# Optimization experiments

Hardware: AMD Instinct MI355X
Metric: run time of the kernel (lower is better)

The kernel has to match this reference:

```python
import jax, jax.numpy as jnp
import numpy as np

B, R, P, DP, DR, N, RK = 4, 256, 64, 384, 512, 48, 24


def _ln(x, w, b, eps=1e-5):
    m = x.mean(-1, keepdims=True)
    v = ((x - m) ** 2).mean(-1, keepdims=True)
    return (x - m) / jnp.sqrt(v + eps) * w + b


def _l2norm(x, eps=1e-6):
    return x / jnp.maximum(jnp.linalg.norm(x, axis=-1, keepdims=True), eps)


def setup_inputs() -> dict:
    key = jax.random.key(0)
    ks = jax.random.split(key, 16)
    s = 0.02
    rnd = lambda k, shp: jax.random.normal(k, shp, jnp.float32) * s
    inp = {
        'patch_tokens': jax.random.normal(ks[0], (B, R, P, DP), jnp.float32),
        'patch_mask': jax.random.randint(ks[1], (B, R, P), 0, 2) > 0,
        'near_mask': jax.random.randint(ks[2], (R, R), 0, 2) > 0,
        'far_mask': jax.random.randint(ks[3], (R, R), 0, 2) > 0,
        'local_pos': rnd(ks[4], (1, 1, P, DP)),
        'gate_ln_w': jnp.ones(DP), 'gate_ln_b': jnp.zeros(DP),
        'gate_w1': rnd(ks[5], (DP, DR)), 'gate_b1': jnp.zeros(DR),
        'gate_w2': rnd(ks[6], (DR, 1)), 'gate_b2': jnp.zeros(1),
        'proj_ln1_w': jnp.ones(DP), 'proj_ln1_b': jnp.zeros(DP),
        'proj_w1': rnd(ks[7], (DP, DR)), 'proj_b1': jnp.zeros(DR),
        'proj_w2': rnd(ks[8], (DR, DR)), 'proj_b2': jnp.zeros(DR),
        'proj_ln2_w': jnp.ones(DR), 'proj_ln2_b': jnp.zeros(DR),
        'in_proj_w': rnd(ks[9], (DR, 2 * DR)),
        'x_proj_w': rnd(ks[10], (DR, RK + 2 * N)),
        'dt_w': rnd(ks[11], (RK, DR)),
        'dt_b': jax.random.uniform(ks[12], (DR,), jnp.float32, -4.0, -2.0),
        'A_log': jnp.tile(jnp.log(jnp.arange(1, N + 1, dtype=jnp.float32))[None, :], (DR, 1)),
        'D_param': jnp.ones(DR),
        'out_proj_w': rnd(ks[13], (DR, DR)),
        'scan_ln_w': jnp.ones(DR), 'scan_ln_b': jnp.zeros(DR),
    }
    return inp


def _forward(patch_tokens, patch_mask, near_mask, far_mask, local_pos,
             gate_ln_w, gate_ln_b, gate_w1, gate_b1, gate_w2, gate_b2,
             proj_ln1_w, proj_ln1_b, proj_w1, proj_b1, proj_w2, proj_b2,
             proj_ln2_w, proj_ln2_b, in_proj_w, x_proj_w, dt_w, dt_b,
             A_log, D_param, out_proj_w, scan_ln_w, scan_ln_b):
    # ---- GatedRegionAggregator ----
    x = patch_tokens + local_pos  # [B,R,P,DP]
    g = _ln(x, gate_ln_w, gate_ln_b)
    g = jax.nn.gelu(g @ gate_w1 + gate_b1, approximate=False)
    logits = (g @ gate_w2 + gate_b2)[..., 0]  # [B,R,P]
    logits = jnp.where(patch_mask, logits, jnp.finfo(logits.dtype).min)
    attn = jax.nn.softmax(logits, axis=-1) * patch_mask
    attn = attn / jnp.maximum(attn.sum(-1, keepdims=True), 1e-6)
    pooled = jnp.einsum('brp,brpd->brd', attn, x)  # [B,R,DP]
    p = _ln(pooled, proj_ln1_w, proj_ln1_b)
    p = jax.nn.gelu(p @ proj_w1 + proj_b1, approximate=False)
    p = _ln(p @ proj_w2 + proj_b2, proj_ln2_w, proj_ln2_b)
    p = jnp.nan_to_num(p, nan=0.0, posinf=1.0, neginf=-1.0)
    region = _l2norm(p)  # [B,R,DR]

    # ---- SlowSelectiveScan1D over region sequence (L = R) ----
    xz = region @ in_proj_w  # [B,L,2*DR]
    u, z = jnp.split(xz, 2, axis=-1)
    prm = u @ x_proj_w  # [B,L,RK+2N]
    dt_raw, Bm, Cm = prm[..., :RK], prm[..., RK:RK + N], prm[..., RK + N:]
    delta = jnp.minimum(jax.nn.softplus(dt_raw @ dt_w + dt_b), 10.0)  # [B,L,DR]
    A = -jnp.minimum(jnp.exp(A_log), 1e4)  # [DR,N]
    dA = jnp.exp(jnp.clip(delta[..., None] * A[None, None], -30.0, 30.0))  # [B,L,DR,N]
    dBu = delta[..., None] * Bm[:, :, None, :] * u[..., None]  # [B,L,DR,N]
    log_cumA = jnp.cumsum(jnp.log(jnp.maximum(dA, 1e-38)), axis=1)
    h = jnp.exp(log_cumA) * jnp.cumsum(dBu * jnp.exp(-log_cumA), axis=1)
    y_seq = jnp.einsum('bln,bldn->bld', Cm, h) + D_param * u
    y = (y_seq * jax.nn.silu(z)) @ out_proj_w
    out = _ln(region + jnp.nan_to_num(y, nan=0.0, posinf=1.0, neginf=-1.0),
              scan_ln_w, scan_ln_b)  # [B,R,DR]

    # ---- topology_loss_static ----
    rt = _l2norm(out.astype(jnp.float32))
    sim = jnp.einsum('brd,bsd->brs', rt, rt)  # [B,R,R]
    near = near_mask.astype(sim.dtype)[None]
    far = far_mask.astype(sim.dtype)[None]
    near_loss = ((1.0 - sim) * near).sum() / jnp.maximum(near.sum(), 1.0)
    far_loss = (jax.nn.relu(sim - 0.2) * far).sum() / jnp.maximum(far.sum(), 1.0)
    return out, near_loss + far_loss


def reference(patch_tokens, patch_mask, near_mask, far_mask, local_pos,
              gate_ln_w, gate_ln_b, gate_w1, gate_b1, gate_w2, gate_b2,
              proj_ln1_w, proj_ln1_b, proj_w1, proj_b1, proj_w2, proj_b2,
              proj_ln2_w, proj_ln2_b, in_proj_w, x_proj_w, dt_w, dt_b,
              A_log, D_param, out_proj_w, scan_ln_w, scan_ln_b):
    return _forward(patch_tokens, patch_mask, near_mask, far_mask, local_pos,
                    gate_ln_w, gate_ln_b, gate_w1, gate_b1, gate_w2, gate_b2,
                    proj_ln1_w, proj_ln1_b, proj_w1, proj_b1, proj_w2, proj_b2,
                    proj_ln2_w, proj_ln2_b, in_proj_w, x_proj_w, dt_w, dt_b,
                    A_log, D_param, out_proj_w, scan_ln_w, scan_ln_b)
```

## Files before the change

kernel.cpp:

```cpp
#include <hip/hip_runtime.h>
#include <hip/hip_bf16.h>
#include <math.h>

#define B_ 4
#define R_ 256
#define P_ 64
#define DP_ 384
#define DR_ 512
#define N_ 48
#define RK_ 24
#define MROWS (B_*R_*P_)
#define REGS  (B_*R_)

typedef unsigned short ushort_t;
typedef __attribute__((ext_vector_type(8))) short bf16x8;
typedef __attribute__((ext_vector_type(4))) float f32x4;

#define GLOAD16(g, l) __builtin_amdgcn_global_load_lds( \
    (const __attribute__((address_space(1))) unsigned int*)(g), \
    (__attribute__((address_space(3))) unsigned int*)(l), 16, 0, 0)

#define OFF_PW1  0
#define OFF_PW2  196608
#define OFF_INPW 458752
#define OFF_XPW  983040
#define OFF_DTW  1044480
#define NW_TOT   1056768

__device__ __forceinline__ float us2f(unsigned short u){
  union { unsigned int i; float f; } x; x.i = ((unsigned int)u) << 16; return x.f;
}
__device__ __forceinline__ unsigned short f2us(float f){
  __hip_bfloat16 h = __float2bfloat16(f);
  return *reinterpret_cast<unsigned short*>(&h);
}
__device__ __forceinline__ float gelu_f(float x){
  float u = x * 0.70710678118654752f;
  float au = fabsf(u);
  float tt = 1.0f / fmaf(0.3275911f, au, 1.0f);
  float poly = tt * fmaf(tt, fmaf(tt, fmaf(tt, fmaf(tt, 1.061405429f, -1.453152027f),
                       1.421413741f), -0.284496736f), 0.254829592f);
  float erfv = 1.0f - poly * __expf(-au * au);
  erfv = (u < 0.f) ? -erfv : erfv;
  return 0.5f * x * (1.0f + erfv);
}
__device__ __forceinline__ float wred_sum(float v){
#pragma unroll
  for (int m = 1; m < 64; m <<= 1) v += __shfl_xor(v, m, 64);
  return v;
}
__device__ __forceinline__ void block_sum4(float v[4], float* s){
  int lane = threadIdx.x & 63, wid = threadIdx.x >> 6;
#pragma unroll
  for (int i = 0; i < 4; ++i){
    float x = v[i];
#pragma unroll
    for (int m = 1; m < 64; m <<= 1) x += __shfl_xor(x, m, 64);
    if (lane == 0) s[wid * 4 + i] = x;
  }
  __syncthreads();
  if (threadIdx.x < 4){
    float t = 0.f;
    for (int t2 = 0; t2 < 8; ++t2) t += s[t2 * 4 + threadIdx.x];
    s[32 + threadIdx.x] = t;
  }
  __syncthreads();
#pragma unroll
  for (int i = 0; i < 4; ++i) v[i] = s[32 + i];
  __syncthreads();
}
__device__ __forceinline__ void block_sum2(float& a, float& b, float* s){
  int lane = threadIdx.x & 63, wid = threadIdx.x >> 6;
  float x = a, y = b;
#pragma unroll
  for (int m = 1; m < 64; m <<= 1){ x += __shfl_xor(x, m, 64); y += __shfl_xor(y, m, 64); }
  if (lane == 0){ s[wid * 2] = x; s[wid * 2 + 1] = y; }
  __syncthreads();
  if (threadIdx.x < 2){
    float t = 0.f;
    for (int j = 0; j < 8; ++j) t += s[j * 2 + threadIdx.x];
    s[16 + threadIdx.x] = t;
  }
  __syncthreads();
  a = s[16]; b = s[17];
  __syncthreads();
}

__global__ __launch_bounds__(512) void k_prep(
    const float* __restrict__ gw1, const float* __restrict__ glnw,
    const float* __restrict__ glnb, const float* __restrict__ gb1,
    ushort_t* __restrict__ W1pT, float* __restrict__ s1,
    float* __restrict__ b1p, float* __restrict__ accum){
  __shared__ float pss[8][64], psb[8][64];
  int tid = threadIdx.x, seg = tid >> 6, nl = tid & 63;
  int n = blockIdx.x * 64 + nl;
  if (blockIdx.x == 0 && tid < 4) accum[tid] = 0.f;
  float s = 0.f, sb = 0.f;
  int k0 = seg * 48;
  for (int i = 0; i < 48; ++i){
    int k = k0 + i;
    float w1 = gw1[k * DR_ + n];
    float v = glnw[k] * w1;
    unsigned short vr = f2us(v);
    s  += us2f(vr);
    sb += glnb[k] * w1;
    W1pT[(size_t)n * DP_ + k] = vr;
  }
  pss[seg][nl] = s; psb[seg][nl] = sb;
  __syncthreads();
  if (tid < 64){
    float ts = 0.f, tb = 0.f;
    for (int j = 0; j < 8; ++j){ ts += pss[j][tid]; tb += psb[j][tid]; }
    s1[blockIdx.x * 64 + tid] = ts;
    b1p[blockIdx.x * 64 + tid] = gb1[blockIdx.x * 64 + tid] + tb;
  }
}

// ... 17 lines not shown
__global__ __launch_bounds__(512) void k_xform(
    const float* __restrict__ pt, const float* __restrict__ lp,
    ushort_t* __restrict__ xb, float* __restrict__ mu, float* __restrict__ rsg){
  int tid = threadIdx.x, w = tid >> 6, lane = tid & 63;
  size_t r = (size_t)blockIdx.x * 8 + w;
  int p = (int)(r & (P_ - 1));
  const float* xr = pt + r * DP_ + lane * 6;
  const float* lr = lp + (size_t)p * DP_ + lane * 6;
  float x[6];
  float s = 0.f, ss = 0.f;
#pragma unroll
  for (int i = 0; i < 6; i += 2){
    float2 a = *(const float2*)(xr + i);
    float2 b = *(const float2*)(lr + i);
    x[i] = a.x + b.x; x[i + 1] = a.y + b.y;
  }
#pragma unroll
  for (int i = 0; i < 6; ++i){ s += x[i]; ss += x[i] * x[i]; }
  s = wred_sum(s); ss = wred_sum(ss);
  if (lane == 0){
    float m = s * (1.f / DP_);
    float var = ss * (1.f / DP_) - m * m;
    mu[r] = m;
    rsg[r] = rsqrtf(var + 1e-5f);
  }
  ushort_t* xw = xb + r * DP_ + lane * 6;
#pragma unroll
  for (int i = 0; i < 6; i += 2){
    ushort2 u2; u2.x = f2us(x[i]); u2.y = f2us(x[i + 1]);
    *(ushort2*)(xw + i) = u2;
  }
}

__global__ __launch_bounds__(1024) void k_gate(
    const ushort_t* __restrict__ xb,
    const ushort_t* __restrict__ BT,
    const float* __restrict__ mu, const float* __restrict__ rsg,
    const float* __restrict__ s1, const float* __restrict__ b1p,
    const float* __restrict__ w2, float* __restrict__ logits){
  __shared__ __align__(16) ushort_t Abuf[2][128 * 64];
  __shared__ float logit_lds[128];
  __shared__ float smu[128], srs[128];
  int tid = threadIdx.x;
  int lane = tid & 63, w = tid >> 6;
  int t = lane & 15, g = lane >> 4;
  long r0 = (long)blockIdx.x * 128;
  if (tid < 128){
    logit_lds[tid] = 0.f;
    smu[tid] = mu[r0 + tid];
    srs[tid] = rsg[r0 + tid];
  }

  f32x4 acc[8][2];
#pragma unroll
  for (int m = 0; m < 8; ++m)
#pragma unroll
    for (int n = 0; n < 2; ++n) acc[m][n] = (f32x4){0.f, 0.f, 0.f, 0.f};

  int ro = lane >> 3, c = lane & 7;
  int srow = (w << 3) + ro;
  const ushort_t* asrc = xb + (size_t)(r0 + srow) * DP_ + ((c ^ (srow & 7)) << 3);

  GLOAD16(asrc, Abuf[0] + (w << 9));
  __syncthreads();

  for (int kt = 0; kt < 6; ++kt){
    int cb = kt & 1;
    if (kt < 5) GLOAD16(asrc + (kt + 1) * 64, Abuf[cb ^ 1] + (w << 9));
    bf16x8 bfr[2][2];
#pragma unroll
    for (int kk = 0; kk < 2; ++kk)
#pragma unroll
      for (int n = 0; n < 2; ++n){
        int col = w * 32 + n * 16 + t;
        bfr[kk][n] = *(const bf16x8*)(BT + (size_t)col * DP_ + kt * 64 + (kk * 4 + g) * 8);
      }
#pragma unroll
    for (int kk = 0; kk < 2; ++kk){
      int ch = kk * 4 + g;
#pragma unroll
      for (int m = 0; m < 8; ++m){
        int row = m * 16 + t;
        bf16x8 af = *(const bf16x8*)(Abuf[cb] + row * 64 + ((ch ^ (row & 7)) << 3));
#pragma unroll
        for (int n = 0; n < 2; ++n)
          acc[m][n] = __builtin_amdgcn_mfma_f32_16x16x32_bf16(af, bfr[kk][n], acc[m][n], 0, 0, 0);
      }
    }
    __syncthreads();
  }

  float w2c[2], s1c[2], b1c[2];
#pragma unroll
  for (int n = 0; n < 2; ++n){
    int col = w * 32 + n * 16 + t;
    w2c[n] = w2[col]; s1c[n] = s1[col]; b1c[n] = b1p[col];
  }
#pragma unroll
  for (int m = 0; m < 8; ++m){
#pragma unroll
    for (int j = 0; j < 4; ++j){
      int rl = m * 16 + g * 4 + j;
      float mur = smu[rl], rs = srs[rl];
      float part = 0.f;
#pragma unroll
      for (int n = 0; n < 2; ++n){
        float gp = rs * acc[m][n][j] - mur * rs * s1c[n] + b1c[n];
        part += gelu_f(gp) * w2c[n];
      }
#pragma unroll
      for (int msk = 1; msk < 16; msk <<= 1) part += __shfl_xor(part, msk, 64);
      if (t == 0) atomicAdd(&logit_lds[rl], part);
    }
  }
  __syncthreads();
  if (tid < 128) logits[r0 + tid] = logit_lds[tid];
}

__global__ __launch_bounds__(512) void k_pool(
    const ushort_t* __restrict__ xb, const float* __restrict__ logits,
    const int* __restrict__ pmask, float* __restrict__ pooled){
  __shared__ float attn[64];
  __shared__ float part[8][DP_];
  int tid = threadIdx.x;
  long r0 = (long)blockIdx.x * 64;
  if (tid < 64){
    int mk = pmask[r0 + tid];
    float lv = logits[r0 + tid];
    float lm = mk ? lv : -3.4e38f;
    float M = lm;
#pragma unroll
    for (int m2 = 1; m2 < 64; m2 <<= 1) M = fmaxf(M, __shfl_xor(M, m2, 64));
    float e = mk ? __expf(lv - M) : 0.f;
    float S = e;
#pragma unroll
    for (int m2 = 1; m2 < 64; m2 <<= 1) S += __shfl_xor(S, m2, 64);
    float a = (S > 0.f) ? e / S : 0.f;
    float S2 = a;
#pragma unroll
    for (int m2 = 1; m2 < 64; m2 <<= 1) S2 += __shfl_xor(S2, m2, 64);
    attn[tid] = a / fmaxf(S2, 1e-6f);
  }
  __syncthreads();
  if (tid < 384){
    int pg = tid / 48, c = tid % 48;
    float acc[8] = {0,0,0,0,0,0,0,0};
#pragma unroll
    for (int i = 0; i < 8; ++i){
      int p = pg + i * 8;
      bf16x8 v = *(const bf16x8*)(xb + (size_t)(r0 + p) * DP_ + c * 8);
      float ap = attn[p];
#pragma unroll
      for (int j = 0; j < 8; ++j) acc[j] = fmaf(ap, us2f((unsigned short)v[j]), acc[j]);
    }
#pragma unroll
    for (int j = 0; j < 8; ++j) part[pg][c * 8 + j] = acc[j];
  }
  __syncthreads();
  if (tid < DP_){
    float s = 0.f;
#pragma unroll
    for (int g2 = 0; g2 < 8; ++g2) s += part[g2][tid];
    pooled[(long)blockIdx.x * DP_ + tid] = s;
  }
}

__global__ __launch_bounds__(512, 4) void k_region(
    const float* __restrict__ pooled,
    const float* __restrict__ ln1w, const float* __restrict__ ln1b,
    const ushort_t* __restrict__ wblob, const float* __restrict__ pb1,
    const float* __restrict__ pb2,
    const float* __restrict__ ln2w, const float* __restrict__ ln2b,
    const float* __restrict__ dtb,
    float* __restrict__ region, float* __restrict__ uT, float* __restrict__ zT,
    float* __restrict__ deltaT, float* __restrict__ BmT, float* __restrict__ CmT){
  const ushort_t* pw1b  = wblob + OFF_PW1;
  const ushort_t* pw2b  = wblob + OFF_PW2;
  const ushort_t* inpwb = wblob + OFF_INPW;
  const ushort_t* xpwb  = wblob + OFF_XPW;
  const ushort_t* dtwb  = wblob + OFF_DTW;
  __shared__ float xr[2][DP_];
  __shared__ float p1[2][DR_];
  __shared__ float rg[2][DR_];
  __shared__ float us[2][DR_];
  __shared__ float ps[4][2][128];
  __shared__ float prm[2][RK_ + 2 * N_];
  __shared__ float red[24];
  int tid = threadIdx.x;
  int r0 = blockIdx.x * 2;
  for (int i = tid; i < 2 * DP_; i += 512) xr[i / DP_][i % DP_] = pooled[(long)r0 * DP_ + i];
  __syncthreads();
  float v0 = (tid < DP_) ? xr[0][tid] : 0.f;
  float v1 = (tid < DP_) ? xr[1][tid] : 0.f;
  float s0 = v0, s1v = v1;
  block_sum2(s0, s1v, red);
  float dv0 = (tid < DP_) ? (v0 - s0 * (1.f / DP_)) : 0.f;
  float dv1 = (tid < DP_) ? (v1 - s1v * (1.f / DP_)) : 0.f;
  float q0 = dv0 * dv0, q1 = dv1 * dv1;
  block_sum2(q0, q1, red);
  if (tid < DP_){
    float lw = ln1w[tid], lb = ln1b[tid];
    xr[0][tid] = dv0 * rsqrtf(q0 * (1.f / DP_) + 1e-5f) * lw + lb;
    xr[1][tid] = dv1 * rsqrtf(q1 * (1.f / DP_) + 1e-5f) * lw + lb;
  }
  __syncthreads();
  {
    float pb = pb1[tid];
    float a0 = pb, a1 = pb;
    for (int k0 = 0; k0 < DP_; k0 += 16){
      ushort_t wv[16];
#pragma unroll
      for (int j = 0; j < 16; ++j) wv[j] = pw1b[(k0 + j) * DR_ + tid];
#pragma unroll
      for (int j = 0; j < 16; ++j){
        float wf = us2f(wv[j]);
        a0 = fmaf(xr[0][k0 + j], wf, a0);
        a1 = fmaf(xr[1][k0 + j], wf, a1);
      }
    }
    p1[0][tid] = gelu_f(a0); p1[1][tid] = gelu_f(a1);
  }
  __syncthreads();
  float qq0, qq1;
  {
    float pb = pb2[tid];
    float a0 = pb, a1 = pb;
    for (int k0 = 0; k0 < DR_; k0 += 16){
      ushort_t wv[16];
#pragma unroll
      for (int j = 0; j < 16; ++j) wv[j] = pw2b[(k0 + j) * DR_ + tid];
#pragma unroll
      for (int j = 0; j < 16; ++j){
        float wf = us2f(wv[j]);
        a0 = fmaf(p1[0][k0 + j], wf, a0);
        a1 = fmaf(p1[1][k0 + j], wf, a1);
      }
    }
    qq0 = a0; qq1 = a1;
  }
  {
    float m0 = qq0, m1 = qq1;
    block_sum2(m0, m1, red);
    float d0 = qq0 - m0 * (1.f / DR_), d1 = qq1 - m1 * (1.f / DR_);
    float w0 = d0 * d0, w1 = d1 * d1;
    block_sum2(w0, w1, red);
    float lw = ln2w[tid], lb = ln2b[tid];
    float o0 = d0 * rsqrtf(w0 * (1.f / DR_) + 1e-5f) * lw + lb;
    float o1 = d1 * rsqrtf(w1 * (1.f / DR_) + 1e-5f) * lw + lb;
    if (isnan(o0)) o0 = 0.f; else if (isinf(o0)) o0 = (o0 > 0.f) ? 1.f : -1.f;
    if (isnan(o1)) o1 = 0.f; else if (isinf(o1)) o1 = (o1 > 0.f) ? 1.f : -1.f;
    float n0 = o0 * o0, n1 = o1 * o1;
    block_sum2(n0, n1, red);
    float r0v = o0 / fmaxf(sqrtf(n0), 1e-6f);
    float r1v = o1 / fmaxf(sqrtf(n1), 1e-6f);
    rg[0][tid] = r0v; rg[1][tid] = r1v;
    region[(long)r0 * DR_ + tid] = r0v;
    region[(long)(r0 + 1) * DR_ + tid] = r1v;
  }
  __syncthreads();
  {
    float ua0 = 0.f, ua1 = 0.f, zb0 = 0.f, zb1 = 0.f;
    for (int k0 = 0; k0 < DR_; k0 += 8){
      ushort_t w1v[8], w2v[8];
#pragma unroll
      for (int j = 0; j < 8; ++j){
        w1v[j] = inpwb[(k0 + j) * 1024 + tid];
        w2v[j] = inpwb[(k0 + j) * 1024 + tid + 512];
      }
#pragma unroll
      for (int j = 0; j < 8; ++j){
        float x0 = rg[0][k0 + j], x1 = rg[1][k0 + j];
        float wa = us2f(w1v[j]), wb = us2f(w2v[j]);
        ua0 = fmaf(x0, wa, ua0); ua1 = fmaf(x1, wa, ua1);
        zb0 = fmaf(x0, wb, zb0); zb1 = fmaf(x1, wb, zb1);
      }
    }
    us[0][tid] = ua0; us[1][tid] = ua1;
    uT[(long)tid * REGS + r0] = ua0;
    uT[(long)tid * REGS + r0 + 1] = ua1;
    zT[(long)tid * REGS + r0] = zb0;
    zT[(long)tid * REGS + r0 + 1] = zb1;
  }
  __syncthreads();
  {
    int sseg = tid >> 7, c = tid & 127;
    float pr0 = 0.f, pr1 = 0.f;
    if (c < RK_ + 2 * N_){
      int kb = sseg * 128;
      for (int k0 = kb; k0 < kb + 128; k0 += 16){
        ushort_t wv[16];
#pragma unroll
        for (int j = 0; j < 16; ++j) wv[j] = xpwb[(k0 + j) * (RK_ + 2 * N_) + c];
#pragma unroll
        for (int j = 0; j < 16; ++j){
          float wf = us2f(wv[j]);
          pr0 = fmaf(us[0][k0 + j], wf, pr0);
          pr1 = fmaf(us[1][k0 + j], wf, pr1);
        }
      }
    }
    ps[sseg][0][c] = pr0; ps[sseg][1][c] = pr1;
  }
  __syncthreads();
  if (tid < 256){
    int rr2 = tid >> 7, cc = tid & 127;
    if (cc < RK_ + 2 * N_)
      prm[rr2][cc] = ps[0][rr2][cc] + ps[1][rr2][cc] + ps[2][rr2][cc] + ps[3][rr2][cc];
  }
  __syncthreads();
#pragma unroll
  for (int r = 0; r < 2; ++r){
    float aa = dtb[tid];
#pragma unroll
    for (int j = 0; j < RK_; ++j) aa = fmaf(prm[r][j], us2f(dtwb[j * DR_ + tid]), aa);
    float sp = (aa > 20.f) ? aa : log1pf(expf(aa));
    deltaT[(long)tid * REGS + r0 + r] = fminf(sp, 10.f);
  }
  if (tid < N_){
#pragma unroll
    for (int r = 0; r < 2; ++r){
      BmT[(long)tid * REGS + r0 + r] = prm[r][RK_ + tid];
      CmT[(long)tid * REGS + r0 + r] = prm[r][RK_ + N_ + tid];
    }
  }
}

__global__ __launch_bounds__(256) void k_scan(
    const float* __restrict__ deltaT, const float* __restrict__ uT,
    const float* __restrict__ zT, const float* __restrict__ BmT,
    const float* __restrict__ CmT, const float* __restrict__ alog,
    const float* __restrict__ Dp, float* __restrict__ ys){
  __shared__ float sAn[N_];
  __shared__ float sA[N_][4];
  __shared__ float sB[N_][4];
  int tid = threadIdx.x, lane = tid & 63, w = tid >> 6;
  int ch = blockIdx.x;
  int b = ch >> 9, d = ch & (DR_ - 1);
  if (tid < N_) sAn[tid] = -fminf(__expf(alog[d * N_ + tid]), 10000.f);
  long col = (long)b * R_ + tid;
  float dl = deltaT[(long)d * REGS + col];
  float uu = uT[(long)d * REGS + col];
  float zz = zT[(long)d * REGS + col];
  float Dd = Dp[d];
  float part = 0.f;
  __syncthreads();
  for (int nc = 0; nc < 6; ++nc){
    float bmv[8], cmv[8];
#pragma unroll
    for (int j = 0; j < 8; ++j){
      bmv[j] = BmT[(long)(nc * 8 + j) * REGS + col];
      cmv[j] = CmT[(long)(nc * 8 + j) * REGS + col];
    }
    float aA[8], aB[8];
// ... 8 lines not shown
        float a_sh = __shfl_up(a, (unsigned)s, 64);
        float b_sh = __shfl_up(bv, (unsigned)s, 64);
        float nb = fmaf(a, b_sh, bv);
        float na = a * a_sh;
        if (lane >= s){ bv = nb; a = na; }
      }
      aA[j] = a; aB[j] = bv;
      if (lane == 63){ sA[n][w] = a; sB[n][w] = bv; }
    }
    __syncthreads();
#pragma unroll
    for (int j = 0; j < 8; ++j){
      int n = nc * 8 + j;
      float hin = 0.f;
#pragma unroll
      for (int tt = 0; tt < 3; ++tt){
        if (tt < w) hin = sA[n][tt] * hin + sB[n][tt];
      }
      float h = fmaf(aA[j], hin, aB[j]);
      part = fmaf(cmv[j], h, part);
    }
    if (nc < 5) __syncthreads();
  }
  float yv = part + Dd * uu;
  float sz = zz / (1.f + __expf(-zz));
  ys[col * DR_ + d] = yv * sz;
}

__global__ __launch_bounds__(512) void k_out(
    const float* __restrict__ ys, const float* __restrict__ W,
    const float* __restrict__ region, const float* __restrict__ lnw,
    const float* __restrict__ lnb, float* __restrict__ outp,
    float* __restrict__ rt){
  __shared__ float yr[4][DR_];
  __shared__ float red[40];
  int tid = threadIdx.x;
  int r0 = blockIdx.x * 4;
  for (int i = tid; i < 4 * DR_; i += 512) yr[i >> 9][i & 511] = ys[(long)r0 * DR_ + i];
  __syncthreads();
  float y[4] = {0,0,0,0};
  for (int k0 = 0; k0 < DR_; k0 += 8){
    float wv[8];
#pragma unroll
    for (int j = 0; j < 8; ++j) wv[j] = W[(k0 + j) * DR_ + tid];
#pragma unroll
    for (int j = 0; j < 8; ++j){
#pragma unroll
      for (int i = 0; i < 4; ++i) y[i] = fmaf(yr[i][k0 + j], wv[j], y[i]);
    }
  }
  float v[4], t4[4];
#pragma unroll
  for (int i = 0; i < 4; ++i){
    if (isnan(y[i])) y[i] = 0.f; else if (isinf(y[i])) y[i] = (y[i] > 0.f) ? 1.f : -1.f;
    v[i] = region[(long)(r0 + i) * DR_ + tid] + y[i];
    t4[i] = v[i];
  }
  block_sum4(t4, red);
  float dv[4];
#pragma unroll
  for (int i = 0; i < 4; ++i){ dv[i] = v[i] - t4[i] * (1.f / DR_); t4[i] = dv[i] * dv[i]; }
  block_sum4(t4, red);
  float o[4];
  float lw = lnw[tid], lb = lnb[tid];
#pragma unroll
  for (int i = 0; i < 4; ++i){
    o[i] = dv[i] * rsqrtf(t4[i] * (1.f / DR_) + 1e-5f) * lw + lb;
    outp[(long)(r0 + i) * DR_ + tid] = o[i];
    t4[i] = o[i] * o[i];
  }
  block_sum4(t4, red);
#pragma unroll
  for (int i = 0; i < 4; ++i)
    rt[(long)(r0 + i) * DR_ + tid] = o[i] / fmaxf(sqrtf(t4[i]), 1e-6f);
}

__global__ __launch_bounds__(512) void k_loss(
    const float* __restrict__ rt, const int* __restrict__ nearm,
    const int* __restrict__ farm, float* __restrict__ accum){
  __shared__ __align__(16) float ar[4][DR_];
  __shared__ float ps[2][4][256];
// ... 57 lines not shown
  const float* glnw  = (const float*)d_in[5];
  const float* glnb  = (const float*)d_in[6];
  const float* gw1   = (const float*)d_in[7];
  const float* gb1   = (const float*)d_in[8];
  const float* gw2   = (const float*)d_in[9];
  const float* pln1w = (const float*)d_in[11];
  const float* pln1b = (const float*)d_in[12];
  const float* pw1   = (const float*)d_in[13];
  const float* pb1   = (const float*)d_in[14];
  const float* pw2   = (const float*)d_in[15];
  const float* pb2   = (const float*)d_in[16];
  const float* pln2w = (const float*)d_in[17];
  const float* pln2b = (const float*)d_in[18];
  const float* inpw  = (const float*)d_in[19];
  const float* xpw   = (const float*)d_in[20];
  const float* dtw   = (const float*)d_in[21];
  const float* dtb   = (const float*)d_in[22];
  const float* alog  = (const float*)d_in[23];
  const float* dpar  = (const float*)d_in[24];
  const float* opw   = (const float*)d_in[25];
  const float* slnw  = (const float*)d_in[26];
  const float* slnb  = (const float*)d_in[27];

  char* ws = (char*)d_ws;
  size_t off = 0;
  auto alloc = [&](size_t bytes){ size_t o = off; off += (bytes + 255) & ~(size_t)255; return o; };
  ushort_t* W1pT  = (ushort_t*)(ws + alloc((size_t)DR_ * DP_ * 2));
  float* s1     = (float*)(ws + alloc(DR_ * 4));
  float* b1p    = (float*)(ws + alloc(DR_ * 4));
  ushort_t* wblob = (ushort_t*)(ws + alloc((size_t)NW_TOT * 2));
  ushort_t* xb  = (ushort_t*)(ws + alloc((size_t)MROWS * DP_ * 2));
  float* mu     = (float*)(ws + alloc((size_t)MROWS * 4));
  float* rsg    = (float*)(ws + alloc((size_t)MROWS * 4));
  float* logits = (float*)(ws + alloc((size_t)MROWS * 4));
  float* pooled = (float*)(ws + alloc((size_t)REGS * DP_ * 4));
  float* region = (float*)(ws + alloc((size_t)REGS * DR_ * 4));
  float* uT     = (float*)(ws + alloc((size_t)REGS * DR_ * 4));
  float* zT     = (float*)(ws + alloc((size_t)REGS * DR_ * 4));
  float* deltaT = (float*)(ws + alloc((size_t)REGS * DR_ * 4));
  float* BmT    = (float*)(ws + alloc((size_t)REGS * N_ * 4));
  float* CmT    = (float*)(ws + alloc((size_t)REGS * N_ * 4));
  float* ys     = (float*)(ws + alloc((size_t)REGS * DR_ * 4));
  float* rt     = (float*)(ws + alloc((size_t)REGS * DR_ * 4));
  float* accum  = (float*)(ws + alloc(4 * 4));

  float* outp = (float*)d_out;

  k_prep<<<dim3(8), dim3(512), 0, stream>>>(gw1, glnw, glnb, gb1, W1pT, s1, b1p, accum);
  k_cast<<<dim3((NW_TOT / 4 + 511) / 512), dim3(512), 0, stream>>>(pw1, pw2, inpw, xpw, dtw, wblob);
  k_xform<<<dim3(MROWS / 8), dim3(512), 0, stream>>>(pt, lp, xb, mu, rsg);
  k_gate<<<dim3(MROWS / 128), dim3(1024), 0, stream>>>(xb, W1pT, mu, rsg, s1, b1p, gw2, logits);
  k_pool<<<dim3(REGS), dim3(512), 0, stream>>>(xb, logits, pmask, pooled);
  k_region<<<dim3(REGS / 2), dim3(512), 0, stream>>>(pooled, pln1w, pln1b, wblob, pb1, pb2, pln2w, pln2b,
                                                     dtb, region, uT, zT, deltaT, BmT, CmT);
  k_scan<<<dim3(B_ * DR_), dim3(256), 0, stream>>>(deltaT, uT, zT, BmT, CmT, alog, dpar, ys);
  k_out<<<dim3(REGS / 4), dim3(512), 0, stream>>>(ys, opw, region, slnw, slnb, outp, rt);
  k_loss<<<dim3(REGS / 4), dim3(512), 0, stream>>>(rt, nearm, farm, accum);
  k_final<<<dim3(1), dim3(64), 0, stream>>>(accum, outp);
}
```

Baseline: 322.8 us.

## Fuse gate and pool kernels, batch four regions in k_region, cheaper GELU

Merges the gate GEMM and the attention pooling into one kernel, so logits stay in LDS instead of making a global round trip and a separate launch. LDS atomics in the gate epilogue become per-wave partial sums followed by a reduction. k_region now handles four regions per block instead of two, halving its grid and reusing each weight load across more rows. The GELU erf approximation drops to a lower-order polynomial, which reduces accuracy.

```diff
diff --git a/kernel.cpp b/kernel.cpp
--- a/kernel.cpp
+++ b/kernel.cpp
@@ -37,9 +37,8 @@
 __device__ __forceinline__ float gelu_f(float x){
   float u = x * 0.70710678118654752f;
   float au = fabsf(u);
-  float tt = 1.0f / fmaf(0.3275911f, au, 1.0f);
-  float poly = tt * fmaf(tt, fmaf(tt, fmaf(tt, fmaf(tt, 1.061405429f, -1.453152027f),
-                       1.421413741f), -0.284496736f), 0.254829592f);
+  float tt = 1.0f / fmaf(0.47047f, au, 1.0f);
+  float poly = tt * fmaf(tt, fmaf(tt, 0.7478556f, -0.0958798f), 0.3480242f);
   float erfv = 1.0f - poly * __expf(-au * au);
   erfv = (u < 0.f) ? -erfv : erfv;
   return 0.5f * x * (1.0f + erfv);
@@ -67,22 +66,6 @@
   __syncthreads();
 #pragma unroll
   for (int i = 0; i < 4; ++i) v[i] = s[32 + i];
-  __syncthreads();
-}
-__device__ __forceinline__ void block_sum2(float& a, float& b, float* s){
-  int lane = threadIdx.x & 63, wid = threadIdx.x >> 6;
-  float x = a, y = b;
-#pragma unroll
-  for (int m = 1; m < 64; m <<= 1){ x += __shfl_xor(x, m, 64); y += __shfl_xor(y, m, 64); }
-  if (lane == 0){ s[wid * 2] = x; s[wid * 2 + 1] = y; }
-  __syncthreads();
-  if (threadIdx.x < 2){
-    float t = 0.f;
-    for (int j = 0; j < 8; ++j) t += s[j * 2 + threadIdx.x];
-    s[16 + threadIdx.x] = t;
-  }
-  __syncthreads();
-  a = s[16]; b = s[17];
   __syncthreads();
 }
 
@@ -166,21 +149,23 @@
   }
 }
 
-__global__ __launch_bounds__(1024) void k_gate(
+__global__ __launch_bounds__(1024, 8) void k_gate_pool(
     const ushort_t* __restrict__ xb,
     const ushort_t* __restrict__ BT,
     const float* __restrict__ mu, const float* __restrict__ rsg,
     const float* __restrict__ s1, const float* __restrict__ b1p,
-    const float* __restrict__ w2, float* __restrict__ logits){
+    const float* __restrict__ w2, const int* __restrict__ pmask,
+    float* __restrict__ pooled){
   __shared__ __align__(16) ushort_t Abuf[2][128 * 64];
+  __shared__ float wpart[16][128];
   __shared__ float logit_lds[128];
   __shared__ float smu[128], srs[128];
+  __shared__ float attn2[2][64];
   int tid = threadIdx.x;
   int lane = tid & 63, w = tid >> 6;
   int t = lane & 15, g = lane >> 4;
   long r0 = (long)blockIdx.x * 128;
   if (tid < 128){
-    logit_lds[tid] = 0.f;
     smu[tid] = mu[r0 + tid];
     srs[tid] = rsg[r0 + tid];
   }
@@ -244,23 +229,23 @@
       }
 #pragma unroll
       for (int msk = 1; msk < 16; msk <<= 1) part += __shfl_xor(part, msk, 64);
-      if (t == 0) atomicAdd(&logit_lds[rl], part);
-    }
-  }
-  __syncthreads();
-  if (tid < 128) logits[r0 + tid] = logit_lds[tid];
-}
-
-__global__ __launch_bounds__(512) void k_pool(
-    const ushort_t* __restrict__ xb, const float* __restrict__ logits,
-    const int* __restrict__ pmask, float* __restrict__ pooled){
-  __shared__ float attn[64];
-  __shared__ float part[8][DP_];
-  int tid = threadIdx.x;
-  long r0 = (long)blockIdx.x * 64;
-  if (tid < 64){
-    int mk = pmask[r0 + tid];
-    float lv = logits[r0 + tid];
+      if (t == 0) wpart[w][rl] = part;
+    }
+  }
+  __syncthreads();
+  if (tid < 128){
+    float s = 0.f;
+#pragma unroll
+    for (int wi = 0; wi < 16; ++wi) s += wpart[wi][tid];
+    logit_lds[tid] = s;
+  }
+  __syncthreads();
+
+  int half = tid >> 9, lt = tid & 511;
+  long rr0 = r0 + half * 64;
+  if (lt < 64){
+    int mk = pmask[rr0 + lt];
+    float lv = logit_lds[half * 64 + lt];
     float lm = mk ? lv : -3.4e38f;
     float M = lm;
 #pragma unroll
@@ -273,29 +258,31 @@
     float S2 = a;
 #pragma unroll
     for (int m2 = 1; m2 < 64; m2 <<= 1) S2 += __shfl_xor(S2, m2, 64);
-    attn[tid] = a / fmaxf(S2, 1e-6f);
-  }
-  __syncthreads();
-  if (tid < 384){
-    int pg = tid / 48, c = tid % 48;
-    float acc[8] = {0,0,0,0,0,0,0,0};
+    attn2[half][lt] = a / fmaxf(S2, 1e-6f);
+  }
+  __syncthreads();
+
+  float* pbuf = (float*)Abuf;
+  if (lt < 384){
+    int pg = lt / 48, cc = lt % 48;
+    float a8[8] = {0,0,0,0,0,0,0,0};
 #pragma unroll
     for (int i = 0; i < 8; ++i){
       int p = pg + i * 8;
-      bf16x8 v = *(const bf16x8*)(xb + (size_t)(r0 + p) * DP_ + c * 8);
-      float ap = attn[p];
-#pragma unroll
-      for (int j = 0; j < 8; ++j) acc[j] = fmaf(ap, us2f((unsigned short)v[j]), acc[j]);
-    }
-#pragma unroll
-    for (int j = 0; j < 8; ++j) part[pg][c * 8 + j] = acc[j];
-  }
-  __syncthreads();
-  if (tid < DP_){
+      bf16x8 v = *(const bf16x8*)(xb + (size_t)(rr0 + p) * DP_ + cc * 8);
+      float ap = attn2[half][p];
+#pragma unroll
+      for (int j = 0; j < 8; ++j) a8[j] = fmaf(ap, us2f((unsigned short)v[j]), a8[j]);
+    }
+#pragma unroll
+    for (int j = 0; j < 8; ++j) pbuf[(half * 8 + pg) * DP_ + cc * 8 + j] = a8[j];
+  }
+  __syncthreads();
+  if (lt < 384){
     float s = 0.f;
 #pragma unroll
-    for (int g2 = 0; g2 < 8; ++g2) s += part[g2][tid];
-    pooled[(long)blockIdx.x * DP_ + tid] = s;
+    for (int g2 = 0; g2 < 8; ++g2) s += pbuf[(half * 8 + g2) * DP_ + lt];
+    pooled[(long)(2 * blockIdx.x + half) * DP_ + lt] = s;
   }
 }
 
@@ -313,34 +300,35 @@
   const ushort_t* inpwb = wblob + OFF_INPW;
   const ushort_t* xpwb  = wblob + OFF_XPW;
   const ushort_t* dtwb  = wblob + OFF_DTW;
-  __shared__ float xr[2][DP_];
-  __shared__ float p1[2][DR_];
-  __shared__ float rg[2][DR_];
-  __shared__ float us[2][DR_];
-  __shared__ float ps[4][2][128];
-  __shared__ float prm[2][RK_ + 2 * N_];
-  __shared__ float red[24];
+  __shared__ float xr[4][DP_];
+  __shared__ float p1[4][DR_];
+  __shared__ float rg[4][DR_];
+  __shared__ float us[4][DR_];
+  __shared__ float ps[4][4][128];
+  __shared__ float prm[4][RK_ + 2 * N_];
+  __shared__ float red[40];
   int tid = threadIdx.x;
-  int r0 = blockIdx.x * 2;
-  for (int i = tid; i < 2 * DP_; i += 512) xr[i / DP_][i % DP_] = pooled[(long)r0 * DP_ + i];
-  __syncthreads();
-  float v0 = (tid < DP_) ? xr[0][tid] : 0.f;
-  float v1 = (tid < DP_) ? xr[1][tid] : 0.f;
-  float s0 = v0, s1v = v1;
-  block_sum2(s0, s1v, red);
-  float dv0 = (tid < DP_) ? (v0 - s0 * (1.f / DP_)) : 0.f;
-  float dv1 = (tid < DP_) ? (v1 - s1v * (1.f / DP_)) : 0.f;
-  float q0 = dv0 * dv0, q1 = dv1 * dv1;
-  block_sum2(q0, q1, red);
+  int r0 = blockIdx.x * 4;
+  for (int i = tid; i < 4 * DP_; i += 512) xr[i / DP_][i % DP_] = pooled[(long)r0 * DP_ + i];
+  __syncthreads();
+  float v[4], t4[4];
+#pragma unroll
+  for (int i = 0; i < 4; ++i){ v[i] = (tid < DP_) ? xr[i][tid] : 0.f; t4[i] = v[i]; }
+  block_sum4(t4, red);
+  float dv[4];
+#pragma unroll
+  for (int i = 0; i < 4; ++i){ dv[i] = (tid < DP_) ? (v[i] - t4[i] * (1.f / DP_)) : 0.f; t4[i] = dv[i] * dv[i]; }
+  block_sum4(t4, red);
   if (tid < DP_){
     float lw = ln1w[tid], lb = ln1b[tid];
-    xr[0][tid] = dv0 * rsqrtf(q0 * (1.f / DP_) + 1e-5f) * lw + lb;
-    xr[1][tid] = dv1 * rsqrtf(q1 * (1.f / DP_) + 1e-5f) * lw + lb;
+#pragma unroll
+    for (int i = 0; i < 4; ++i)
+      xr[i][tid] = dv[i] * rsqrtf(t4[i] * (1.f / DP_) + 1e-5f) * lw + lb;
   }
   __syncthreads();
   {
     float pb = pb1[tid];
-    float a0 = pb, a1 = pb;
+    float a[4] = {pb, pb, pb, pb};
     for (int k0 = 0; k0 < DP_; k0 += 16){
       ushort_t wv[16];
 #pragma unroll
@@ -348,17 +336,18 @@
 #pragma unroll
       for (int j = 0; j < 16; ++j){
         float wf = us2f(wv[j]);
-        a0 = fmaf(xr[0][k0 + j], wf, a0);
-        a1 = fmaf(xr[1][k0 + j], wf, a1);
-      }
-    }
-    p1[0][tid] = gelu_f(a0); p1[1][tid] = gelu_f(a1);
-  }
-  __syncthreads();
-  float qq0, qq1;
+#pragma unroll
+        for (int i = 0; i < 4; ++i) a[i] = fmaf(xr[i][k0 + j], wf, a[i]);
+      }
+    }
+#pragma unroll
+    for (int i = 0; i < 4; ++i) p1[i][tid] = gelu_f(a[i]);
+  }
+  __syncthreads();
+  float qq[4];
   {
     float pb = pb2[tid];
-    float a0 = pb, a1 = pb;
+    float a[4] = {pb, pb, pb, pb};
     for (int k0 = 0; k0 < DR_; k0 += 16){
       ushort_t wv[16];
 #pragma unroll
@@ -366,34 +355,40 @@
 #pragma unroll
       for (int j = 0; j < 16; ++j){
         float wf = us2f(wv[j]);
-        a0 = fmaf(p1[0][k0 + j], wf, a0);
-        a1 = fmaf(p1[1][k0 + j], wf, a1);
-      }
-    }
-    qq0 = a0; qq1 = a1;
+#pragma unroll
+        for (int i = 0; i < 4; ++i) a[i] = fmaf(p1[i][k0 + j], wf, a[i]);
+      }
+    }
+#pragma unroll
+    for (int i = 0; i < 4; ++i) qq[i] = a[i];
   }
   {
-    float m0 = qq0, m1 = qq1;
-    block_sum2(m0, m1, red);
-    float d0 = qq0 - m0 * (1.f / DR_), d1 = qq1 - m1 * (1.f / DR_);
-    float w0 = d0 * d0, w1 = d1 * d1;
-    block_sum2(w0, w1, red);
+#pragma unroll
+    for (int i = 0; i < 4; ++i) t4[i] = qq[i];
+    block_sum4(t4, red);
+    float d2[4];
+#pragma unroll
+    for (int i = 0; i < 4; ++i){ d2[i] = qq[i] - t4[i] * (1.f / DR_); t4[i] = d2[i] * d2[i]; }
+    block_sum4(t4, red);
     float lw = ln2w[tid], lb = ln2b[tid];
-    float o0 = d0 * rsqrtf(w0 * (1.f / DR_) + 1e-5f) * lw + lb;
-    float o1 = d1 * rsqrtf(w1 * (1.f / DR_) + 1e-5f) * lw + lb;
-    if (isnan(o0)) o0 = 0.f; else if (isinf(o0)) o0 = (o0 > 0.f) ? 1.f : -1.f;
-    if (isnan(o1)) o1 = 0.f; else if (isinf(o1)) o1 = (o1 > 0.f) ? 1.f : -1.f;
-    float n0 = o0 * o0, n1 = o1 * o1;
-    block_sum2(n0, n1, red);
-    float r0v = o0 / fmaxf(sqrtf(n0), 1e-6f);
-    float r1v = o1 / fmaxf(sqrtf(n1), 1e-6f);
-    rg[0][tid] = r0v; rg[1][tid] = r1v;
-    region[(long)r0 * DR_ + tid] = r0v;
-    region[(long)(r0 + 1) * DR_ + tid] = r1v;
+    float o[4];
+#pragma unroll
+    for (int i = 0; i < 4; ++i){
+      o[i] = d2[i] * rsqrtf(t4[i] * (1.f / DR_) + 1e-5f) * lw + lb;
+      if (isnan(o[i])) o[i] = 0.f; else if (isinf(o[i])) o[i] = (o[i] > 0.f) ? 1.f : -1.f;
+      t4[i] = o[i] * o[i];
+    }
+    block_sum4(t4, red);
+#pragma unroll
+    for (int i = 0; i < 4; ++i){
+      float rv = o[i] / fmaxf(sqrtf(t4[i]), 1e-6f);
+      rg[i][tid] = rv;
+      region[(long)(r0 + i) * DR_ + tid] = rv;
+    }
   }
   __syncthreads();
   {
-    float ua0 = 0.f, ua1 = 0.f, zb0 = 0.f, zb1 = 0.f;
+    float ua[4] = {0,0,0,0}, zb[4] = {0,0,0,0};
     for (int k0 = 0; k0 < DR_; k0 += 8){
       ushort_t w1v[8], w2v[8];
 #pragma unroll
@@ -403,47 +398,51 @@
       }
 #pragma unroll
       for (int j = 0; j < 8; ++j){
-        float x0 = rg[0][k0 + j], x1 = rg[1][k0 + j];
         float wa = us2f(w1v[j]), wb = us2f(w2v[j]);
-        ua0 = fmaf(x0, wa, ua0); ua1 = fmaf(x1, wa, ua1);
-        zb0 = fmaf(x0, wb, zb0); zb1 = fmaf(x1, wb, zb1);
-      }
-    }
-    us[0][tid] = ua0; us[1][tid] = ua1;
-    uT[(long)tid * REGS + r0] = ua0;
-    uT[(long)tid * REGS + r0 + 1] = ua1;
-    zT[(long)tid * REGS + r0] = zb0;
-    zT[(long)tid * REGS + r0 + 1] = zb1;
+#pragma unroll
+        for (int i = 0; i < 4; ++i){
+          float x = rg[i][k0 + j];
+          ua[i] = fmaf(x, wa, ua[i]); zb[i] = fmaf(x, wb, zb[i]);
+        }
+      }
+    }
+#pragma unroll
+    for (int i = 0; i < 4; ++i){
+      us[i][tid] = ua[i];
+      uT[(long)tid * REGS + r0 + i] = ua[i];
+      zT[(long)tid * REGS + r0 + i] = zb[i];
+    }
   }
   __syncthreads();
   {
-    int sseg = tid >> 7, c = tid & 127;
-    float pr0 = 0.f, pr1 = 0.f;
-    if (c < RK_ + 2 * N_){
+    int sseg = tid >> 7, cc = tid & 127;
+    float pr[4] = {0,0,0,0};
+    if (cc < RK_ + 2 * N_){
       int kb = sseg * 128;
       for (int k0 = kb; k0 < kb + 128; k0 += 16){
         ushort_t wv[16];
 #pragma unroll
-        for (int j = 0; j < 16; ++j) wv[j] = xpwb[(k0 + j) * (RK_ + 2 * N_) + c];
+        for (int j = 0; j < 16; ++j) wv[j] = xpwb[(k0 + j) * (RK_ + 2 * N_) + cc];
 #pragma unroll
         for (int j = 0; j < 16; ++j){
           float wf = us2f(wv[j]);
-          pr0 = fmaf(us[0][k0 + j], wf, pr0);
-          pr1 = fmaf(us[1][k0 + j], wf, pr1);
+#pragma unroll
+          for (int i = 0; i < 4; ++i) pr[i] = fmaf(us[i][k0 + j], wf, pr[i]);
         }
       }
     }
-    ps[sseg][0][c] = pr0; ps[sseg][1][c] = pr1;
-  }
-  __syncthreads();
-  if (tid < 256){
+#pragma unroll
+    for (int i = 0; i < 4; ++i) ps[sseg][i][cc] = pr[i];
+  }
+  __syncthreads();
+  {
     int rr2 = tid >> 7, cc = tid & 127;
     if (cc < RK_ + 2 * N_)
       prm[rr2][cc] = ps[0][rr2][cc] + ps[1][rr2][cc] + ps[2][rr2][cc] + ps[3][rr2][cc];
   }
   __syncthreads();
 #pragma unroll
-  for (int r = 0; r < 2; ++r){
+  for (int r = 0; r < 4; ++r){
     float aa = dtb[tid];
 #pragma unroll
     for (int j = 0; j < RK_; ++j) aa = fmaf(prm[r][j], us2f(dtwb[j * DR_ + tid]), aa);
@@ -452,7 +451,7 @@
   }
   if (tid < N_){
 #pragma unroll
-    for (int r = 0; r < 2; ++r){
+    for (int r = 0; r < 4; ++r){
       BmT[(long)tid * REGS + r0 + r] = prm[r][RK_ + tid];
       CmT[(long)tid * REGS + r0 + r] = prm[r][RK_ + N_ + tid];
     }
@@ -665,7 +664,6 @@
   ushort_t* xb  = (ushort_t*)(ws + alloc((size_t)MROWS * DP_ * 2));
   float* mu     = (float*)(ws + alloc((size_t)MROWS * 4));
   float* rsg    = (float*)(ws + alloc((size_t)MROWS * 4));
-  float* logits = (float*)(ws + alloc((size_t)MROWS * 4));
   float* pooled = (float*)(ws + alloc((size_t)REGS * DP_ * 4));
   float* region = (float*)(ws + alloc((size_t)REGS * DR_ * 4));
   float* uT     = (float*)(ws + alloc((size_t)REGS * DR_ * 4));
@@ -682,9 +680,8 @@
   k_prep<<<dim3(8), dim3(512), 0, stream>>>(gw1, glnw, glnb, gb1, W1pT, s1, b1p, accum);
   k_cast<<<dim3((NW_TOT / 4 + 511) / 512), dim3(512), 0, stream>>>(pw1, pw2, inpw, xpw, dtw, wblob);
   k_xform<<<dim3(MROWS / 8), dim3(512), 0, stream>>>(pt, lp, xb, mu, rsg);
-  k_gate<<<dim3(MROWS / 128), dim3(1024), 0, stream>>>(xb, W1pT, mu, rsg, s1, b1p, gw2, logits);
-  k_pool<<<dim3(REGS), dim3(512), 0, stream>>>(xb, logits, pmask, pooled);
-  k_region<<<dim3(REGS / 2), dim3(512), 0, stream>>>(pooled, pln1w, pln1b, wblob, pb1, pb2, pln2w, pln2b,
+  k_gate_pool<<<dim3(MROWS / 128), dim3(1024), 0, stream>>>(xb, W1pT, mu, rsg, s1, b1p, gw2, pmask, pooled);
+  k_region<<<dim3(REGS / 4), dim3(512), 0, stream>>>(pooled, pln1w, pln1b, wblob, pb1, pb2, pln2w, pln2b,
                                                      dtb, region, uT, zT, deltaT, BmT, CmT);
   k_scan<<<dim3(B_ * DR_), dim3(256), 0, stream>>>(deltaT, uT, zT, BmT, CmT, alog, dpar, ys);
   k_out<<<dim3(REGS / 4), dim3(512), 0, stream>>>(ys, opw, region, slnw, slnb, outp, rt);
```

Result: slower. 597.4 us (+85.0%).

## Fuse gate and pool kernels, use cheaper GELU erf, vectorize LDS reads

Applied to the files above, without the earlier changes.

Merges k_gate and k_pool into one kernel. Each 128-row tile now does the attention softmax and weighted pooling for its two regions directly, so the logits round trip and one launch go away, and the LDS atomics are replaced by per-wave partial sums. The GELU erf approximation changes from a 5-term to a 3-term Abramowitz-Stegun polynomial, which costs accuracy. Matvec loops in k_region and k_out now read LDS activations as float4, and launch bounds ask for more occupancy.

```diff
diff --git a/kernel.cpp b/kernel.cpp
--- a/kernel.cpp
+++ b/kernel.cpp
@@ -37,9 +37,8 @@
 __device__ __forceinline__ float gelu_f(float x){
   float u = x * 0.70710678118654752f;
   float au = fabsf(u);
-  float tt = 1.0f / fmaf(0.3275911f, au, 1.0f);
-  float poly = tt * fmaf(tt, fmaf(tt, fmaf(tt, fmaf(tt, 1.061405429f, -1.453152027f),
-                       1.421413741f), -0.284496736f), 0.254829592f);
+  float tt = 1.0f / fmaf(0.47047f, au, 1.0f);
+  float poly = tt * fmaf(tt, fmaf(tt, 0.7478556f, -0.0958798f), 0.3480242f);
   float erfv = 1.0f - poly * __expf(-au * au);
   erfv = (u < 0.f) ? -erfv : erfv;
   return 0.5f * x * (1.0f + erfv);
@@ -166,21 +165,23 @@
   }
 }
 
-__global__ __launch_bounds__(1024) void k_gate(
+__global__ __launch_bounds__(1024, 4) void k_gate_pool(
     const ushort_t* __restrict__ xb,
     const ushort_t* __restrict__ BT,
     const float* __restrict__ mu, const float* __restrict__ rsg,
     const float* __restrict__ s1, const float* __restrict__ b1p,
-    const float* __restrict__ w2, float* __restrict__ logits){
+    const float* __restrict__ w2, const int* __restrict__ pmask,
+    float* __restrict__ pooled){
   __shared__ __align__(16) ushort_t Abuf[2][128 * 64];
+  __shared__ float wpart[16][128];
   __shared__ float logit_lds[128];
   __shared__ float smu[128], srs[128];
+  __shared__ float attn2[2][64];
   int tid = threadIdx.x;
   int lane = tid & 63, w = tid >> 6;
   int t = lane & 15, g = lane >> 4;
   long r0 = (long)blockIdx.x * 128;
   if (tid < 128){
-    logit_lds[tid] = 0.f;
     smu[tid] = mu[r0 + tid];
     srs[tid] = rsg[r0 + tid];
   }
@@ -244,23 +245,23 @@
       }
 #pragma unroll
       for (int msk = 1; msk < 16; msk <<= 1) part += __shfl_xor(part, msk, 64);
-      if (t == 0) atomicAdd(&logit_lds[rl], part);
-    }
-  }
-  __syncthreads();
-  if (tid < 128) logits[r0 + tid] = logit_lds[tid];
-}
-
-__global__ __launch_bounds__(512) void k_pool(
-    const ushort_t* __restrict__ xb, const float* __restrict__ logits,
-    const int* __restrict__ pmask, float* __restrict__ pooled){
-  __shared__ float attn[64];
-  __shared__ float part[8][DP_];
-  int tid = threadIdx.x;
-  long r0 = (long)blockIdx.x * 64;
-  if (tid < 64){
-    int mk = pmask[r0 + tid];
-    float lv = logits[r0 + tid];
+      if (t == 0) wpart[w][rl] = part;
+    }
+  }
+  __syncthreads();
+  if (tid < 128){
+    float s = 0.f;
+#pragma unroll
+    for (int wi = 0; wi < 16; ++wi) s += wpart[wi][tid];
+    logit_lds[tid] = s;
+  }
+  __syncthreads();
+
+  int half = tid >> 9, lt = tid & 511;
+  long rr0 = r0 + half * 64;
+  if (lt < 64){
+    int mk = pmask[rr0 + lt];
+    float lv = logit_lds[half * 64 + lt];
     float lm = mk ? lv : -3.4e38f;
     float M = lm;
 #pragma unroll
@@ -273,29 +274,31 @@
     float S2 = a;
 #pragma unroll
     for (int m2 = 1; m2 < 64; m2 <<= 1) S2 += __shfl_xor(S2, m2, 64);
-    attn[tid] = a / fmaxf(S2, 1e-6f);
-  }
-  __syncthreads();
-  if (tid < 384){
-    int pg = tid / 48, c = tid % 48;
-    float acc[8] = {0,0,0,0,0,0,0,0};
+    attn2[half][lt] = a / fmaxf(S2, 1e-6f);
+  }
+  __syncthreads();
+
+  float* pbuf = (float*)Abuf;
+  if (lt < 384){
+    int pg = lt / 48, cc = lt % 48;
+    float a8[8] = {0,0,0,0,0,0,0,0};
 #pragma unroll
     for (int i = 0; i < 8; ++i){
       int p = pg + i * 8;
-      bf16x8 v = *(const bf16x8*)(xb + (size_t)(r0 + p) * DP_ + c * 8);
-      float ap = attn[p];
-#pragma unroll
-      for (int j = 0; j < 8; ++j) acc[j] = fmaf(ap, us2f((unsigned short)v[j]), acc[j]);
-    }
-#pragma unroll
-    for (int j = 0; j < 8; ++j) part[pg][c * 8 + j] = acc[j];
-  }
-  __syncthreads();
-  if (tid < DP_){
+      bf16x8 v = *(const bf16x8*)(xb + (size_t)(rr0 + p) * DP_ + cc * 8);
+      float ap = attn2[half][p];
+#pragma unroll
+      for (int j = 0; j < 8; ++j) a8[j] = fmaf(ap, us2f((unsigned short)v[j]), a8[j]);
+    }
+#pragma unroll
+    for (int j = 0; j < 8; ++j) pbuf[(half * 8 + pg) * DP_ + cc * 8 + j] = a8[j];
+  }
+  __syncthreads();
+  if (lt < 384){
     float s = 0.f;
 #pragma unroll
-    for (int g2 = 0; g2 < 8; ++g2) s += part[g2][tid];
-    pooled[(long)blockIdx.x * DP_ + tid] = s;
+    for (int g2 = 0; g2 < 8; ++g2) s += pbuf[(half * 8 + g2) * DP_ + lt];
+    pooled[(long)(2 * blockIdx.x + half) * DP_ + lt] = s;
   }
 }
 
@@ -313,10 +316,10 @@
   const ushort_t* inpwb = wblob + OFF_INPW;
   const ushort_t* xpwb  = wblob + OFF_XPW;
   const ushort_t* dtwb  = wblob + OFF_DTW;
-  __shared__ float xr[2][DP_];
-  __shared__ float p1[2][DR_];
-  __shared__ float rg[2][DR_];
-  __shared__ float us[2][DR_];
+  __shared__ __align__(16) float xr[2][DP_];
+  __shared__ __align__(16) float p1[2][DR_];
+  __shared__ __align__(16) float rg[2][DR_];
+  __shared__ __align__(16) float us[2][DR_];
   __shared__ float ps[4][2][128];
   __shared__ float prm[2][RK_ + 2 * N_];
   __shared__ float red[24];
@@ -346,10 +349,15 @@
 #pragma unroll
       for (int j = 0; j < 16; ++j) wv[j] = pw1b[(k0 + j) * DR_ + tid];
 #pragma unroll
-      for (int j = 0; j < 16; ++j){
-        float wf = us2f(wv[j]);
-        a0 = fmaf(xr[0][k0 + j], wf, a0);
-        a1 = fmaf(xr[1][k0 + j], wf, a1);
+      for (int j4 = 0; j4 < 16; j4 += 4){
+        float4 x0 = *(const float4*)(&xr[0][k0 + j4]);
+        float4 x1 = *(const float4*)(&xr[1][k0 + j4]);
+        float w0 = us2f(wv[j4]), w1f = us2f(wv[j4 + 1]);
+        float w2f = us2f(wv[j4 + 2]), w3 = us2f(wv[j4 + 3]);
+        a0 = fmaf(x0.x, w0, a0); a1 = fmaf(x1.x, w0, a1);
+        a0 = fmaf(x0.y, w1f, a0); a1 = fmaf(x1.y, w1f, a1);
+        a0 = fmaf(x0.z, w2f, a0); a1 = fmaf(x1.z, w2f, a1);
+        a0 = fmaf(x0.w, w3, a0); a1 = fmaf(x1.w, w3, a1);
       }
     }
     p1[0][tid] = gelu_f(a0); p1[1][tid] = gelu_f(a1);
@@ -364,10 +372,15 @@
 #pragma unroll
       for (int j = 0; j < 16; ++j) wv[j] = pw2b[(k0 + j) * DR_ + tid];
 #pragma unroll
-      for (int j = 0; j < 16; ++j){
-        float wf = us2f(wv[j]);
-        a0 = fmaf(p1[0][k0 + j], wf, a0);
-        a1 = fmaf(p1[1][k0 + j], wf, a1);
+      for (int j4 = 0; j4 < 16; j4 += 4){
+        float4 x0 = *(const float4*)(&p1[0][k0 + j4]);
+        float4 x1 = *(const float4*)(&p1[1][k0 + j4]);
+        float w0 = us2f(wv[j4]), w1f = us2f(wv[j4 + 1]);
+        float w2f = us2f(wv[j4 + 2]), w3 = us2f(wv[j4 + 3]);
+        a0 = fmaf(x0.x, w0, a0); a1 = fmaf(x1.x, w0, a1);
+        a0 = fmaf(x0.y, w1f, a0); a1 = fmaf(x1.y, w1f, a1);
+        a0 = fmaf(x0.z, w2f, a0); a1 = fmaf(x1.z, w2f, a1);
+        a0 = fmaf(x0.w, w3, a0); a1 = fmaf(x1.w, w3, a1);
       }
     }
     qq0 = a0; qq1 = a1;
@@ -402,11 +415,17 @@
         w2v[j] = inpwb[(k0 + j) * 1024 + tid + 512];
       }
 #pragma unroll
-      for (int j = 0; j < 8; ++j){
-        float x0 = rg[0][k0 + j], x1 = rg[1][k0 + j];
-        float wa = us2f(w1v[j]), wb = us2f(w2v[j]);
-        ua0 = fmaf(x0, wa, ua0); ua1 = fmaf(x1, wa, ua1);
-        zb0 = fmaf(x0, wb, zb0); zb1 = fmaf(x1, wb, zb1);
+      for (int j4 = 0; j4 < 8; j4 += 4){
+        float4 x0 = *(const float4*)(&rg[0][k0 + j4]);
+        float4 x1 = *(const float4*)(&rg[1][k0 + j4]);
+        float xs0[4] = {x0.x, x0.y, x0.z, x0.w};
+        float xs1[4] = {x1.x, x1.y, x1.z, x1.w};
+#pragma unroll
+        for (int j = 0; j < 4; ++j){
+          float wa = us2f(w1v[j4 + j]), wb = us2f(w2v[j4 + j]);
+          ua0 = fmaf(xs0[j], wa, ua0); ua1 = fmaf(xs1[j], wa, ua1);
+          zb0 = fmaf(xs0[j], wb, zb0); zb1 = fmaf(xs1[j], wb, zb1);
+        }
       }
     }
     us[0][tid] = ua0; us[1][tid] = ua1;
@@ -426,10 +445,15 @@
 #pragma unroll
         for (int j = 0; j < 16; ++j) wv[j] = xpwb[(k0 + j) * (RK_ + 2 * N_) + c];
 #pragma unroll
-        for (int j = 0; j < 16; ++j){
-          float wf = us2f(wv[j]);
-          pr0 = fmaf(us[0][k0 + j], wf, pr0);
-          pr1 = fmaf(us[1][k0 + j], wf, pr1);
+        for (int j4 = 0; j4 < 16; j4 += 4){
+          float4 x0 = *(const float4*)(&us[0][k0 + j4]);
+          float4 x1 = *(const float4*)(&us[1][k0 + j4]);
+          float w0 = us2f(wv[j4]), w1f = us2f(wv[j4 + 1]);
+          float w2f = us2f(wv[j4 + 2]), w3 = us2f(wv[j4 + 3]);
+          pr0 = fmaf(x0.x, w0, pr0); pr1 = fmaf(x1.x, w0, pr1);
+          pr0 = fmaf(x0.y, w1f, pr0); pr1 = fmaf(x1.y, w1f, pr1);
+          pr0 = fmaf(x0.z, w2f, pr0); pr1 = fmaf(x1.z, w2f, pr1);
+          pr0 = fmaf(x0.w, w3, pr0); pr1 = fmaf(x1.w, w3, pr1);
         }
       }
     }
@@ -527,7 +551,7 @@
     const float* __restrict__ region, const float* __restrict__ lnw,
     const float* __restrict__ lnb, float* __restrict__ outp,
     float* __restrict__ rt){
-  __shared__ float yr[4][DR_];
+  __shared__ __align__(16) float yr[4][DR_];
   __shared__ float red[40];
   int tid = threadIdx.x;
   int r0 = blockIdx.x * 4;
@@ -539,9 +563,15 @@
 #pragma unroll
     for (int j = 0; j < 8; ++j) wv[j] = W[(k0 + j) * DR_ + tid];
 #pragma unroll
-    for (int j = 0; j < 8; ++j){
-#pragma unroll
-      for (int i = 0; i < 4; ++i) y[i] = fmaf(yr[i][k0 + j], wv[j], y[i]);
+    for (int j4 = 0; j4 < 8; j4 += 4){
+#pragma unroll
+      for (int i = 0; i < 4; ++i){
+        float4 x = *(const float4*)(&yr[i][k0 + j4]);
+        y[i] = fmaf(x.x, wv[j4], y[i]);
+        y[i] = fmaf(x.y, wv[j4 + 1], y[i]);
+        y[i] = fmaf(x.z, wv[j4 + 2], y[i]);
+        y[i] = fmaf(x.w, wv[j4 + 3], y[i]);
+      }
     }
   }
   float v[4], t4[4];
@@ -665,7 +695,6 @@
   ushort_t* xb  = (ushort_t*)(ws + alloc((size_t)MROWS * DP_ * 2));
   float* mu     = (float*)(ws + alloc((size_t)MROWS * 4));
   float* rsg    = (float*)(ws + alloc((size_t)MROWS * 4));
-  float* logits = (float*)(ws + alloc((size_t)MROWS * 4));
   float* pooled = (float*)(ws + alloc((size_t)REGS * DP_ * 4));
   float* region = (float*)(ws + alloc((size_t)REGS * DR_ * 4));
   float* uT     = (float*)(ws + alloc((size_t)REGS * DR_ * 4));
@@ -682,8 +711,7 @@
   k_prep<<<dim3(8), dim3(512), 0, stream>>>(gw1, glnw, glnb, gb1, W1pT, s1, b1p, accum);
   k_cast<<<dim3((NW_TOT / 4 + 511) / 512), dim3(512), 0, stream>>>(pw1, pw2, inpw, xpw, dtw, wblob);
   k_xform<<<dim3(MROWS / 8), dim3(512), 0, stream>>>(pt, lp, xb, mu, rsg);
-  k_gate<<<dim3(MROWS / 128), dim3(1024), 0, stream>>>(xb, W1pT, mu, rsg, s1, b1p, gw2, logits);
-  k_pool<<<dim3(REGS), dim3(512), 0, stream>>>(xb, logits, pmask, pooled);
+  k_gate_pool<<<dim3(MROWS / 128), dim3(1024), 0, stream>>>(xb, W1pT, mu, rsg, s1, b1p, gw2, pmask, pooled);
   k_region<<<dim3(REGS / 2), dim3(512), 0, stream>>>(pooled, pln1w, pln1b, wblob, pb1, pb2, pln2w, pln2b,
                                                      dtb, region, uT, zT, deltaT, BmT, CmT);
   k_scan<<<dim3(B_ * DR_), dim3(256), 0, stream>>>(deltaT, uT, zT, BmT, CmT, alog, dpar, ys);
```

New measurement: 314.7 us. 1.03x faster.
